# Kernel optimization log

Hardware: AMD Instinct MI355X
Metric: run time of the kernel (lower is better)

## Reference

```python
import jax, jax.numpy as jnp
import numpy as np

B, NQ, L, E, K = 64, 1024, 128, 8192, 2
LN_EPS = 1e-5


def setup_inputs() -> dict:
    key = jax.random.key(0)
    ks = jax.random.split(key, 16)
    s1 = 1.0 / np.sqrt(2 * L + 1)
    s2 = 1.0 / np.sqrt(L)
    s3 = 1.0 / np.sqrt(2 * L)
    return {
        "z0": jax.random.normal(ks[0], (B, L), jnp.float32),
        "edge_index": jax.random.randint(ks[1], (2, E), 0, NQ, jnp.int64),
        "edge_attr": jax.random.normal(ks[2], (E,), jnp.float32),
        "n_qubits": NQ,
        # edge MLP params, stacked over K message-passing rounds
        "e_w1": jax.random.normal(ks[3], (K, L, 2 * L + 1), jnp.float32) * s1,
        "e_b1": jnp.zeros((K, L), jnp.float32),
        "e_w2": jax.random.normal(ks[4], (K, L, L), jnp.float32) * s2,
        "e_b2": jnp.zeros((K, L), jnp.float32),
        # node MLP params
        "n_w1": jax.random.normal(ks[5], (K, L, 2 * L), jnp.float32) * s3,
        "n_b1": jnp.zeros((K, L), jnp.float32),
        "ln_g": jnp.ones((K, L), jnp.float32),
        "ln_b": jnp.zeros((K, L), jnp.float32),
        "n_w2": jax.random.normal(ks[6], (K, L, L), jnp.float32) * s2,
        "n_b2": jnp.zeros((K, L), jnp.float32),
    }


def reference(z0, edge_index, edge_attr, n_qubits,
              e_w1, e_b1, e_w2, e_b2,
              n_w1, n_b1, ln_g, ln_b, n_w2, n_b2):
    b, l = z0.shape
    src, tgt = edge_index[0], edge_index[1]
    e_ = src.shape[0]
    # broadcast latent z0 to every node: h [B, N, L]
    h = jnp.broadcast_to(z0[:, None, :], (b, n_qubits, l))
    e = jnp.broadcast_to(edge_attr[None, :, None], (b, e_, 1))  # [B, E, 1]
    k_rounds = e_w1.shape[0]
    for k in range(k_rounds):
        hi = h[:, src, :]  # gather source node feats [B, E, L]
        hj = h[:, tgt, :]  # gather target node feats [B, E, L]
        inp_e = jnp.concatenate([hi, hj, e], axis=-1)  # [B, E, 2L+1]
        m = jax.nn.relu(inp_e @ e_w1[k].T + e_b1[k]) @ e_w2[k].T + e_b2[k]
        # scatter_add messages back to source nodes
        m_agg = jnp.zeros_like(h).at[:, src, :].add(m)
        inp_n = jnp.concatenate([h, m_agg], axis=-1)  # [B, N, 2L]
        x = jax.nn.relu(inp_n @ n_w1[k].T + n_b1[k])
        mu = x.mean(axis=-1, keepdims=True)
        var = ((x - mu) ** 2).mean(axis=-1, keepdims=True)
        x = (x - mu) * jax.lax.rsqrt(var + LN_EPS) * ln_g[k] + ln_b[k]
        # Dropout(p=0.1) is identity in eval mode
        h = x @ n_w2[k].T + n_b2[k] + h  # residual
    return h.mean(axis=1)  # [B, L]
```

## Files before the change

### kernel.cpp

```cpp
#include <hip/hip_runtime.h>

#define B_   64
#define NQ_  1024
#define L_   128
#define E_   8192
#define M_   (B_*NQ_)
#define LDP  136
#define TILE 2176

typedef unsigned short u16;
typedef unsigned int   u32;
typedef __attribute__((ext_vector_type(8))) short short8;
typedef __attribute__((ext_vector_type(4))) float floatx4;

#define WVB() __builtin_amdgcn_wave_barrier()

__device__ __forceinline__ u16 f2bf(float f) {
    union { float f; u32 u; } v; v.f = f;
    return (u16)((v.u + 0x7fffu + ((v.u >> 16) & 1u)) >> 16);
}
__device__ __forceinline__ float bf2f(u16 u) {
    union { u32 u; float f; } v; v.u = ((u32)u) << 16;
    return v.f;
}
__device__ __forceinline__ floatx4 mfma16(short8 a, short8 b, floatx4 c) {
    return __builtin_amdgcn_mfma_f32_16x16x32_bf16(a, b, c, 0, 0, 0);
}
__device__ __forceinline__ short8 gfrag(const u16* base, int r0, int kb, int lane) {
    return *(const short8*)(base + (size_t)(r0 + (lane & 15)) * 128 + kb * 32 + (lane >> 4) * 8);
}
__device__ __forceinline__ short8 sfrag(const u16* t, int r0, int kb, int lane) {
    return *(const short8*)(t + (r0 + (lane & 15)) * LDP + kb * 32 + (lane >> 4) * 8);
}
__device__ __forceinline__ short8 wfrag(const u16* wf, int nt, int kb, int lane) {
    return *(const short8*)(wf + (((kb << 3) + nt) * 64 + lane) * 8);
}
__device__ __forceinline__ void frag_flush(const u16* t, u16* wf, int nt, int lane) {
#pragma unroll
    for (int kb = 0; kb < 4; ++kb)
        *(short8*)(wf + (((kb << 3) + nt) * 64 + lane) * 8) = sfrag(t, 0, kb, lane);
}
__device__ __forceinline__ short8 frag_cvt(const float* base, int r0, int ld, int kb, int lane) {
    const float* p = base + (size_t)(r0 + (lane & 15)) * ld + kb * 32 + (lane >> 4) * 8;
    short8 s;
#pragma unroll
    for (int j = 0; j < 8; ++j) s[j] = (short)f2bf(p[j]);
    return s;
}
__device__ __forceinline__ void tile_store(u16* t, const floatx4* acc, int lane) {
    int col = lane & 15, qd = lane >> 4;
#pragma unroll
    for (int nt = 0; nt < 8; ++nt)
#pragma unroll
        for (int r = 0; r < 4; ++r)
            t[(qd * 4 + r) * LDP + nt * 16 + col] = f2bf(acc[nt][r]);
}
__device__ __forceinline__ void tile_flush(const u16* t, u16* g, int lane) {
#pragma unroll
    for (int it = 0; it < 4; ++it) {
        int chunk = it * 64 + lane, row = chunk >> 4, c8 = chunk & 15;
        *(uint4*)(g + (size_t)row * 128 + c8 * 8) = *(const uint4*)(t + row * LDP + c8 * 8);
    }
}

struct P {
    const int* ei; const float* attr; const float* z0;
    const float* e_w1; const float* e_b1; const float* e_w2; const float* e_b2;
    const float* n_w1; const float* n_b1; const float* ln_g; const float* ln_b;
    const float* n_w2; const float* n_b2;
    int* ofs; int* tgt_s; float* a_s; float* degf;
    u16* wf;
    u16* w_n20;
    float* wl; float* vb2;
    float* rx; float* rci; float* rcj; float* rh; float* mx0;
    u16* c0t; u16* S; u16* t1g; u16* ci1; u16* cj1;
    float* out;
};

__global__ __launch_bounds__(256) void k_setup(P p) {
    __shared__ __align__(16) char smem[17408];
    int tid = threadIdx.x, blk = blockIdx.x;
    int lane = tid & 63, w = tid >> 6, col = lane & 15, qd = lane >> 4;

    if (blk == 0) {
        __shared__ int cnt[1024];
        __shared__ int wsum[4];
        __shared__ int flag;
#pragma unroll
        for (int i = 0; i < 4; ++i) cnt[tid + i * 256] = 0;
        if (tid == 0) flag = 1;
        __syncthreads();
        if (tid < 100 && p.ei[2 * tid + 1] != 0) atomicAnd(&flag, 0);
        __syncthreads();
        int i64 = flag;
        for (int e = tid; e < E_; e += 256) {
            int s = i64 ? p.ei[2 * e] : p.ei[e];
            atomicAdd(&cnt[s], 1);
        }
        __syncthreads();
        int q0 = tid * 4;
        int c0 = cnt[q0], c1 = cnt[q0 + 1], c2 = cnt[q0 + 2], c3 = cnt[q0 + 3];
        int tsum = c0 + c1 + c2 + c3, incl = tsum;
#pragma unroll
        for (int o = 1; o < 64; o <<= 1) {
            int t = __shfl_up(incl, o, 64);
            if (lane >= o) incl += t;
        }
        if (lane == 63) wsum[w] = incl;
        __syncthreads();
        int wo = 0;
        for (int i = 0; i < w; ++i) wo += wsum[i];
        int base = wo + incl - tsum;
        p.ofs[q0] = base; p.ofs[q0 + 1] = base + c0;
        p.ofs[q0 + 2] = base + c0 + c1; p.ofs[q0 + 3] = base + c0 + c1 + c2;
        p.degf[q0] = (float)c0; p.degf[q0 + 1] = (float)c1;
        p.degf[q0 + 2] = (float)c2; p.degf[q0 + 3] = (float)c3;
        if (tid == 0) p.ofs[NQ_] = E_;
        __syncthreads();
        cnt[q0] = base; cnt[q0 + 1] = base + c0;
        cnt[q0 + 2] = base + c0 + c1; cnt[q0 + 3] = base + c0 + c1 + c2;
        __syncthreads();
        for (int e = tid; e < E_; e += 256) {
            int s = i64 ? p.ei[2 * e]        : p.ei[e];
            int t = i64 ? p.ei[2 * (E_ + e)] : p.ei[E_ + e];
            int pos = atomicAdd(&cnt[s], 1);
            p.tgt_s[pos] = t;
            p.a_s[pos]   = p.attr[e];
        }
    } else if (blk <= 2) {
        int base = (blk - 1) * 8192;
        for (int idx = tid; idx < 8192; idx += 256)
            p.w_n20[base + idx] = f2bf(p.n_w2[base + idx]);
    } else if (blk == 3) {
        const float* src = p.n_w2 + 16384;
        u16* dst = p.wf + 5 * 16384;
        for (int pr = w; pr < 32; pr += 4) {
            int kb = pr >> 3, nt = pr & 7;
            const float* s = src + (nt * 16 + col) * 128 + kb * 32 + qd * 8;
            short8 v;
#pragma unroll
            for (int j = 0; j < 8; ++j) v[j] = (short)f2bf(s[j]);
            *(short8*)(dst + (pr * 64 + lane) * 8) = v;
        }
    } else if (blk <= 13) {
        int g = (blk - 4) >> 1, part = (blk - 4) & 1;
        const float* Pm; const float* Q; int ldp; u16* D;
        switch (g) {
            case 0:  Pm = p.n_w1 + 128;             ldp = 256; Q = p.e_w2;         D = p.wf;             break;
            case 1:  Pm = p.n_w1 + 32768 + 128;     ldp = 256; Q = p.e_w2 + 16384; D = p.wf + 4 * 16384; break;
            case 2:  Pm = p.e_w1 + 128 * 257;       ldp = 257; Q = p.n_w2;         D = p.wf + 1 * 16384; break;
            case 3:  Pm = p.e_w1 + 128 * 257 + 128; ldp = 257; Q = p.n_w2;         D = p.wf + 2 * 16384; break;
            default: Pm = p.n_w1 + 32768;           ldp = 256; Q = p.n_w2;         D = p.wf + 3 * 16384; break;
        }
        int tile = part * 4 + w;
        int r0 = tile * 16;
        floatx4 acc[8] = {};
#pragma unroll
        for (int kb = 0; kb < 4; ++kb) {
            short8 a = frag_cvt(Pm, r0, ldp, kb, lane);
#pragma unroll
            for (int nt = 0; nt < 8; ++nt) {
                short8 bq;
#pragma unroll
                for (int j = 0; j < 8; ++j)
                    bq[j] = (short)f2bf(Q[(kb * 32 + qd * 8 + j) * 128 + nt * 16 + col]);
                acc[nt] = mfma16(a, bq, acc[nt]);
            }
        }
        u16* slot = (u16*)smem + w * TILE;
        tile_store(slot, acc, lane); WVB();
        frag_flush(slot, D, tile, lane);
    } else if (blk == 14) {
        int r0 = w * 16;
        floatx4 acc[8] = {};
#pragma unroll
        for (int kb = 0; kb < 4; ++kb) {
            short8 a = frag_cvt(p.z0, r0, 128, kb, lane);
#pragma unroll
            for (int nt = 0; nt < 8; ++nt)
                acc[nt] = mfma16(a, frag_cvt(p.n_w1, nt * 16, 256, kb, lane), acc[nt]);
        }
#pragma unroll
        for (int nt = 0; nt < 8; ++nt) {
            int cg = nt * 16 + col; float bv = p.n_b1[cg];
#pragma unroll
            for (int r = 0; r < 4; ++r) p.rx[(r0 + qd * 4 + r) * 128 + cg] = acc[nt][r] + bv;
        }
    } else if (blk <= 17) {
        int r0 = w * 16;
        const float* Wp; int ld; const float* bias; float* dst;
        if (blk == 15)      { Wp = p.e_w1 + 128 * 257;       ld = 257; bias = p.e_b1 + 128; dst = p.rci; }
        else if (blk == 16) { Wp = p.e_w1 + 128 * 257 + 128; ld = 257; bias = nullptr;      dst = p.rcj; }
        else                { Wp = p.n_w1 + 32768;           ld = 256; bias = p.n_b1 + 128; dst = p.rh;  }
        floatx4 acc[8] = {};
#pragma unroll
        for (int kb = 0; kb < 4; ++kb) {
            short8 a;
            int rr = (r0 + col) * 128, kk = kb * 32 + qd * 8;
#pragma unroll
            for (int j = 0; j < 8; ++j) a[j] = (short)f2bf(p.z0[rr + kk + j] + p.n_b2[kk + j]);
#pragma unroll
            for (int nt = 0; nt < 8; ++nt)
                acc[nt] = mfma16(a, frag_cvt(Wp, nt * 16, ld, kb, lane), acc[nt]);
        }
#pragma unroll
        for (int nt = 0; nt < 8; ++nt) {
            int cg = nt * 16 + col;
            float bv = bias ? bias[cg] : 0.0f;
#pragma unroll
            for (int r = 0; r < 4; ++r) dst[(r0 + qd * 4 + r) * 128 + cg] = acc[nt][r] + bv;
        }
    } else if (blk == 18) {
        int r0 = w * 16;
        floatx4 a1[8] = {};
#pragma unroll
        for (int kb = 0; kb < 4; ++kb) {
            short8 a = frag_cvt(p.z0, r0, 128, kb, lane);
#pragma unroll
            for (int nt = 0; nt < 8; ++nt) {
                a1[nt] = mfma16(a, frag_cvt(p.e_w1,       nt * 16, 257, kb, lane), a1[nt]);
                a1[nt] = mfma16(a, frag_cvt(p.e_w1 + 128, nt * 16, 257, kb, lane), a1[nt]);
            }
        }
#pragma unroll
        for (int nt = 0; nt < 8; ++nt) {
            float bv = p.e_b1[nt * 16 + col];
#pragma unroll
            for (int r = 0; r < 4; ++r) a1[nt][r] += bv;
        }
        u16* slot = (u16*)smem + w * TILE;
        tile_store(slot, a1, lane); WVB();
        tile_flush(slot, p.c0t + (size_t)r0 * 128, lane);
    } else {
        int k = tid >> 7, c = tid & 127;
        const float4* wp = (const float4*)(p.n_w1 + k * 32768 + c * 256 + 128);
        const float4* bp = (const float4*)(p.e_b2 + k * 128);
        float s0 = 0.f, s1 = 0.f, s2 = 0.f, s3 = 0.f;
#pragma unroll
        for (int n4 = 0; n4 < 32; ++n4) {
            float4 a = wp[n4], bv = bp[n4];
            s0 += a.x * bv.x; s1 += a.y * bv.y; s2 += a.z * bv.z; s3 += a.w * bv.w;
        }
        p.vb2[tid] = (s0 + s1) + (s2 + s3);
        p.wl[tid]  = p.e_w1[k * 128 * 257 + c * 257 + 256];
        for (int i = tid; i < 8192; i += 256) p.mx0[i] = 0.0f;
    }
}

__global__ __launch_bounds__(256) void k_edge(P p, int r0) {
    int tid = threadIdx.x, lane = tid & 63, w = tid >> 6;
    const float* wl = r0 ? p.wl : p.wl + 128;
    float2 wl2 = ((const float2*)wl)[lane];
    int gw = blockIdx.x * 4 + w;
    int q = gw & (NQ_ - 1), bg = gw >> 10;
    int bl[8];
#pragma unroll
    for (int i = 0; i < 4; ++i) { bl[i] = bg * 4 + i; bl[i + 4] = bg * 4 + i + 32; }
    int st = p.ofs[q], en = p.ofs[q + 1];
    float ax[8] = {}, ay[8] = {};
    if (r0) {
        float cx[8], cy[8];
#pragma unroll
        for (int i = 0; i < 8; ++i) {
            u32 cv = ((const u32*)p.c0t)[(size_t)bl[i] * 64 + lane];
            cx[i] = bf2f((u16)(cv & 0xffff)); cy[i] = bf2f((u16)(cv >> 16));
        }
        for (int idx = st; idx < en; ++idx) {
            float a = p.a_s[idx];
            float wx = a * wl2.x, wy = a * wl2.y;
#pragma unroll
            for (int i = 0; i < 8; ++i) {
                ax[i] += fmaxf(cx[i] + wx, 0.f);
                ay[i] += fmaxf(cy[i] + wy, 0.f);
            }
        }
    } else {
        const u32* cjp[8];
        float cx[8], cy[8];
#pragma unroll
        for (int i = 0; i < 8; ++i) {
            cjp[i] = (const u32*)p.cj1 + (size_t)bl[i] * NQ_ * 64;
            u32 cv = ((const u32*)p.ci1)[((size_t)bl[i] * NQ_ + q) * 64 + lane];
            cx[i] = bf2f((u16)(cv & 0xffff)); cy[i] = bf2f((u16)(cv >> 16));
        }
        for (int idx = st; idx < en; ++idx) {
            int t = p.tgt_s[idx];
            float a = p.a_s[idx];
            size_t ro = (size_t)t * 64 + lane;
            float wx = a * wl2.x, wy = a * wl2.y;
#pragma unroll
            for (int i = 0; i < 8; ++i) {
                u32 jv = cjp[i][ro];
                ax[i] += fmaxf(cx[i] + bf2f((u16)(jv & 0xffff)) + wx, 0.f);
                ay[i] += fmaxf(cy[i] + bf2f((u16)(jv >> 16))    + wy, 0.f);
            }
        }
    }
    u32* Sp = (u32*)p.S;
#pragma unroll
    for (int i = 0; i < 8; ++i)
        Sp[((size_t)bl[i] * NQ_ + q) * 64 + lane] =
            (u32)f2bf(ax[i]) | ((u32)f2bf(ay[i]) << 16);
}

__global__ __launch_bounds__(256, 2) void k_node0(P p) {
    __shared__ __align__(16) char smem[52224];
    u16* xt = (u16*)smem;
    u16* ob = (u16*)(smem + 34816);
    int tid = threadIdx.x, lane = tid & 63, w = tid >> 6;
    int col = lane & 15, qd = lane >> 4;
    int blk = blockIdx.x;
    int rowbase = blk * 128 + w * 32;
    int b = blk >> 3;

    floatx4 xa[2][8] = {};
#pragma unroll
    for (int kb = 0; kb < 4; ++kb) {
        short8 Bv[8];
#pragma unroll
        for (int nt = 0; nt < 8; ++nt) Bv[nt] = wfrag(p.wf, nt, kb, lane);
#pragma unroll
        for (int t = 0; t < 2; ++t) {
            short8 a = gfrag(p.S, rowbase + t * 16, kb, lane);
#pragma unroll
            for (int nt = 0; nt < 8; ++nt) xa[t][nt] = mfma16(a, Bv[nt], xa[t][nt]);
        }
    }
    float s8[8] = {};
#pragma unroll
    for (int t = 0; t < 2; ++t) {
#pragma unroll
        for (int nt = 0; nt < 8; ++nt) {
            int cg = nt * 16 + col;
            float base = p.rx[b * 128 + cg], vb = p.vb2[cg];
#pragma unroll
            for (int r = 0; r < 4; ++r) {
                int row = rowbase + t * 16 + qd * 4 + r;
                xa[t][nt][r] = fmaxf(xa[t][nt][r] + base + p.degf[row & (NQ_ - 1)] * vb, 0.f);
            }
        }
#pragma unroll
        for (int r = 0; r < 4; ++r) {
            float s = 0.f, s2 = 0.f;
#pragma unroll
            for (int nt = 0; nt < 8; ++nt) { float v = xa[t][nt][r]; s += v; s2 += v * v; }
#pragma unroll
            for (int o = 1; o < 16; o <<= 1) { s += __shfl_xor(s, o, 64); s2 += __shfl_xor(s2, o, 64); }
            float mu = s * (1.f / 128.f), var = s2 * (1.f / 128.f) - mu * mu;
            float rs = rsqrtf(var + 1e-5f);
#pragma unroll
            for (int nt = 0; nt < 8; ++nt) {
                int cg = nt * 16 + col;
                float xv = (xa[t][nt][r] - mu) * rs * p.ln_g[cg] + p.ln_b[cg];
                xa[t][nt][r] = xv;
                s8[nt] += xv;
            }
        }
        tile_store(xt + (w * 2 + t) * TILE, xa[t], lane);
    }
#pragma unroll
    for (int nt = 0; nt < 8; ++nt) {
        s8[nt] += __shfl_xor(s8[nt], 16, 64);
        s8[nt] += __shfl_xor(s8[nt], 32, 64);
    }
    if (lane < 16) {
#pragma unroll
        for (int nt = 0; nt < 8; ++nt)
            atomicAdd(p.mx0 + b * 128 + nt * 16 + lane, s8[nt]);
    }
    WVB();
#pragma unroll
    for (int ph = 0; ph < 3; ++ph) {
        const u16* wfp = p.wf + ((ph == 0) ? 1 : (ph == 1) ? 2 : 3) * 16384;
        const float* rt = (ph == 0) ? p.rci : (ph == 1) ? p.rcj : p.rh;
        floatx4 ca[2][8] = {};
#pragma unroll
        for (int kb = 0; kb < 4; ++kb) {
            short8 Bv[8];
#pragma unroll
            for (int nt = 0; nt < 8; ++nt) Bv[nt] = wfrag(wfp, nt, kb, lane);
#pragma unroll
            for (int t = 0; t < 2; ++t) {
                short8 a = sfrag(xt + (w * 2 + t) * TILE, 0, kb, lane);
#pragma unroll
                for (int nt = 0; nt < 8; ++nt) ca[t][nt] = mfma16(a, Bv[nt], ca[t][nt]);
            }
        }
#pragma unroll
        for (int t = 0; t < 2; ++t)
#pragma unroll
            for (int nt = 0; nt < 8; ++nt) {
                float rc = rt[b * 128 + nt * 16 + col];
#pragma unroll
                for (int r = 0; r < 4; ++r) ca[t][nt][r] += rc;
            }
        u16* dst = (ph == 0) ? p.ci1 : (ph == 1) ? p.cj1 : p.t1g;
#pragma unroll
        for (int t = 0; t < 2; ++t) {
            tile_store(ob + w * TILE, ca[t], lane);
            WVB();
            tile_flush(ob + w * TILE, dst + (size_t)(rowbase + t * 16) * 128, lane);
            WVB();
        }
    }
}

__global__ __launch_bounds__(256, 2) void k_node1(P p) {
    __shared__ __align__(16) char smem[52224];
    u16* ob = (u16*)(smem + 34816);
    int tid = threadIdx.x, lane = tid & 63, w = tid >> 6;
    int col = lane & 15, qd = lane >> 4;
    int blk = blockIdx.x;
    int rowbase = blk * 128 + w * 32;
    int b = blk >> 3;

    const u16* wc1 = p.wf + 4 * 16384;
    floatx4 xa[2][8] = {};
#pragma unroll
    for (int kb = 0; kb < 4; ++kb) {
        short8 Bv[8];
#pragma unroll
        for (int nt = 0; nt < 8; ++nt) Bv[nt] = wfrag(wc1, nt, kb, lane);
#pragma unroll
        for (int t = 0; t < 2; ++t) {
            short8 a = gfrag(p.S, rowbase + t * 16, kb, lane);
#pragma unroll
            for (int nt = 0; nt < 8; ++nt) xa[t][nt] = mfma16(a, Bv[nt], xa[t][nt]);
        }
    }
    const float* vb21 = p.vb2 + 128;
#pragma unroll
    for (int t = 0; t < 2; ++t) {
#pragma unroll
        for (int nt = 0; nt < 8; ++nt) {
            int cg = nt * 16 + col;
            float vb = vb21[cg];
#pragma unroll
            for (int r = 0; r < 4; ++r) {
                int row = rowbase + t * 16 + qd * 4 + r;
                float tv = bf2f(p.t1g[(size_t)row * 128 + cg]);
                xa[t][nt][r] = fmaxf(xa[t][nt][r] + tv + p.degf[row & (NQ_ - 1)] * vb, 0.f);
            }
        }
#pragma unroll
        for (int r = 0; r < 4; ++r) {
            float s = 0.f, s2 = 0.f;
#pragma unroll
            for (int nt = 0; nt < 8; ++nt) { float v = xa[t][nt][r]; s += v; s2 += v * v; }
#pragma unroll
            for (int o = 1; o < 16; o <<= 1) { s += __shfl_xor(s, o, 64); s2 += __shfl_xor(s2, o, 64); }
            float mu = s * (1.f / 128.f), var = s2 * (1.f / 128.f) - mu * mu;
            float rs = rsqrtf(var + 1e-5f);
#pragma unroll
            for (int nt = 0; nt < 8; ++nt) {
                int cg = nt * 16 + col;
                xa[t][nt][r] = (xa[t][nt][r] - mu) * rs * p.ln_g[128 + cg] + p.ln_b[128 + cg];
            }
        }
    }
    const u16* n21 = p.wf + 5 * 16384;
    float s8[8] = {};
#pragma unroll
    for (int t = 0; t < 2; ++t) {
        WVB();
        tile_store(ob + w * TILE, xa[t], lane);
        WVB();
        floatx4 ma[8] = {};
#pragma unroll
        for (int kb = 0; kb < 4; ++kb) {
            short8 Bv[8];
#pragma unroll
            for (int nt = 0; nt < 8; ++nt) Bv[nt] = wfrag(n21, nt, kb, lane);
            short8 a = sfrag(ob + w * TILE, 0, kb, lane);
#pragma unroll
            for (int nt = 0; nt < 8; ++nt) ma[nt] = mfma16(a, Bv[nt], ma[nt]);
        }
#pragma unroll
        for (int nt = 0; nt < 8; ++nt)
#pragma unroll
            for (int r = 0; r < 4; ++r) s8[nt] += ma[nt][r];
    }
#pragma unroll
    for (int nt = 0; nt < 8; ++nt) {
        s8[nt] += __shfl_xor(s8[nt], 16, 64);
        s8[nt] += __shfl_xor(s8[nt], 32, 64);
    }
    if (lane < 16) {
#pragma unroll
        for (int nt = 0; nt < 8; ++nt)
            atomicAdd(p.out + b * 128 + nt * 16 + lane, s8[nt] * (1.f / 1024.f));
    }
    if ((blk & 7) == 0 && tid < 128) {
        int c = tid;
        const float* mx = p.mx0 + b * 128;
        float s = 0.f;
#pragma unroll
        for (int k8 = 0; k8 < 16; ++k8) {
            short8 wv = *(const short8*)(p.w_n20 + c * 128 + k8 * 8);
            const float* mxp = mx + k8 * 8;
#pragma unroll
            for (int j = 0; j < 8; ++j) s += mxp[j] * bf2f((u16)wv[j]);
        }
        float acc = p.z0[b * 128 + c] + p.n_b2[c] + p.n_b2[128 + c] + s * (1.f / 1024.f);
        atomicAdd(p.out + b * 128 + c, acc);
    }
}

extern "C" void kernel_launch(void* const* d_in, const int* in_sizes, int n_in,
                              void* d_out, int out_size, void* d_ws, size_t ws_size,
                              hipStream_t stream) {
    P p;
    p.z0   = (const float*)d_in[0];
    p.ei   = (const int*)d_in[1];
    p.attr = (const float*)d_in[2];
    p.e_w1 = (const float*)d_in[4];
    p.e_b1 = (const float*)d_in[5];
    p.e_w2 = (const float*)d_in[6];
    p.e_b2 = (const float*)d_in[7];
    p.n_w1 = (const float*)d_in[8];
    p.n_b1 = (const float*)d_in[9];
    p.ln_g = (const float*)d_in[10];
    p.ln_b = (const float*)d_in[11];
    p.n_w2 = (const float*)d_in[12];
    p.n_b2 = (const float*)d_in[13];
    p.out  = (float*)d_out;

    const size_t H = (size_t)M_ * L_;
    float* f  = (float*)d_ws;
    p.degf = f;
    p.a_s  = f + 1024;
    p.wl   = p.a_s + 8192;
    p.vb2  = p.wl + 256;
    p.rx   = p.vb2 + 256;
    p.rci  = p.rx + 8192;
    p.rcj  = p.rci + 8192;
    p.rh   = p.rcj + 8192;
    p.mx0  = p.rh + 8192;
    p.ofs  = (int*)(p.mx0 + 8192);
    p.tgt_s = p.ofs + 1056;
    p.wf    = (u16*)(p.tgt_s + 8192);
    p.w_n20 = p.wf + 6 * 16384;
    p.c0t   = p.w_n20 + 16384;
    p.S     = p.c0t + 8192;
    p.t1g   = p.S + H;
    p.ci1   = p.t1g + H;
    p.cj1   = p.ci1 + H;

    hipMemsetAsync(p.out, 0, 8192 * sizeof(float), stream);

    k_setup<<<20, 256, 0, stream>>>(p);
    k_edge<<<2048, 256, 0, stream>>>(p, 1);
    k_node0<<<512, 256, 0, stream>>>(p);
    k_edge<<<2048, 256, 0, stream>>>(p, 0);
    k_node1<<<512, 256, 0, stream>>>(p);
}
```

Before: 188.9 us.

## Fuse edge aggregation into node kernels via LDS tiles, drop S buffer

The separate edge-message kernels are removed. Each node kernel now computes the per-node edge aggregates for its own rows directly into shared-memory tiles, and the MFMA reads its A operand from those tiles instead of a global S buffer. This removes two launches and a full write plus read of the S intermediate. The t1 buffer is also stored in MFMA fragment order, so node1 can load it with packed 64-bit loads. In exchange, the node kernels do serial gather work per wave before the MFMA, with predicated loops padded to the largest degree among the four nodes handled together, and the batch-sharing of loads that the old edge kernel had is lost.

```diff
diff --git a/kernel.cpp b/kernel.cpp
--- a/kernel.cpp
+++ b/kernel.cpp
@@ -10,10 +10,13 @@
 
 typedef unsigned short u16;
 typedef unsigned int   u32;
+typedef unsigned long long u64;
 typedef __attribute__((ext_vector_type(8))) short short8;
 typedef __attribute__((ext_vector_type(4))) float floatx4;
 
 #define WVB() __builtin_amdgcn_wave_barrier()
+
+__device__ __forceinline__ int imax2(int a, int b) { return a > b ? a : b; }
 
 __device__ __forceinline__ u16 f2bf(float f) {
     union { float f; u32 u; } v; v.f = f;
@@ -25,9 +28,6 @@
 }
 __device__ __forceinline__ floatx4 mfma16(short8 a, short8 b, floatx4 c) {
     return __builtin_amdgcn_mfma_f32_16x16x32_bf16(a, b, c, 0, 0, 0);
-}
-__device__ __forceinline__ short8 gfrag(const u16* base, int r0, int kb, int lane) {
-    return *(const short8*)(base + (size_t)(r0 + (lane & 15)) * 128 + kb * 32 + (lane >> 4) * 8);
 }
 __device__ __forceinline__ short8 sfrag(const u16* t, int r0, int kb, int lane) {
     return *(const short8*)(t + (r0 + (lane & 15)) * LDP + kb * 32 + (lane >> 4) * 8);
@@ -73,7 +73,7 @@
     u16* w_n20;
     float* wl; float* vb2;
     float* rx; float* rci; float* rcj; float* rh; float* mx0;
-    u16* c0t; u16* S; u16* t1g; u16* ci1; u16* cj1;
+    u16* c0t; u16* t1g; u16* ci1; u16* cj1;
     float* out;
 };
 
@@ -247,62 +247,6 @@
     }
 }
 
-__global__ __launch_bounds__(256) void k_edge(P p, int r0) {
-    int tid = threadIdx.x, lane = tid & 63, w = tid >> 6;
-    const float* wl = r0 ? p.wl : p.wl + 128;
-    float2 wl2 = ((const float2*)wl)[lane];
-    int gw = blockIdx.x * 4 + w;
-    int q = gw & (NQ_ - 1), bg = gw >> 10;
-    int bl[8];
-#pragma unroll
-    for (int i = 0; i < 4; ++i) { bl[i] = bg * 4 + i; bl[i + 4] = bg * 4 + i + 32; }
-    int st = p.ofs[q], en = p.ofs[q + 1];
-    float ax[8] = {}, ay[8] = {};
-    if (r0) {
-        float cx[8], cy[8];
-#pragma unroll
-        for (int i = 0; i < 8; ++i) {
-            u32 cv = ((const u32*)p.c0t)[(size_t)bl[i] * 64 + lane];
-            cx[i] = bf2f((u16)(cv & 0xffff)); cy[i] = bf2f((u16)(cv >> 16));
-        }
-        for (int idx = st; idx < en; ++idx) {
-            float a = p.a_s[idx];
-            float wx = a * wl2.x, wy = a * wl2.y;
-#pragma unroll
-            for (int i = 0; i < 8; ++i) {
-                ax[i] += fmaxf(cx[i] + wx, 0.f);
-                ay[i] += fmaxf(cy[i] + wy, 0.f);
-            }
-        }
-    } else {
-        const u32* cjp[8];
-        float cx[8], cy[8];
-#pragma unroll
-        for (int i = 0; i < 8; ++i) {
-            cjp[i] = (const u32*)p.cj1 + (size_t)bl[i] * NQ_ * 64;
-            u32 cv = ((const u32*)p.ci1)[((size_t)bl[i] * NQ_ + q) * 64 + lane];
-            cx[i] = bf2f((u16)(cv & 0xffff)); cy[i] = bf2f((u16)(cv >> 16));
-        }
-        for (int idx = st; idx < en; ++idx) {
-            int t = p.tgt_s[idx];
-            float a = p.a_s[idx];
-            size_t ro = (size_t)t * 64 + lane;
-            float wx = a * wl2.x, wy = a * wl2.y;
-#pragma unroll
-            for (int i = 0; i < 8; ++i) {
-                u32 jv = cjp[i][ro];
-                ax[i] += fmaxf(cx[i] + bf2f((u16)(jv & 0xffff)) + wx, 0.f);
-                ay[i] += fmaxf(cy[i] + bf2f((u16)(jv >> 16))    + wy, 0.f);
-            }
-        }
-    }
-    u32* Sp = (u32*)p.S;
-#pragma unroll
-    for (int i = 0; i < 8; ++i)
-        Sp[((size_t)bl[i] * NQ_ + q) * 64 + lane] =
-            (u32)f2bf(ax[i]) | ((u32)f2bf(ay[i]) << 16);
-}
-
 __global__ __launch_bounds__(256, 2) void k_node0(P p) {
     __shared__ __align__(16) char smem[52224];
     u16* xt = (u16*)smem;
@@ -313,6 +257,43 @@
     int rowbase = blk * 128 + w * 32;
     int b = blk >> 3;
 
+    {
+        u32 cv = ((const u32*)p.c0t)[b * 64 + lane];
+        float cx = bf2f((u16)(cv & 0xffffu)), cy = bf2f((u16)(cv >> 16));
+        float2 wl2 = ((const float2*)p.wl)[lane];
+        for (int qq = 0; qq < 32; qq += 4) {
+            int st[4], en[4];
+            float ax[4] = {}, ay[4] = {};
+#pragma unroll
+            for (int j = 0; j < 4; ++j) {
+                int q = (rowbase + qq + j) & (NQ_ - 1);
+                st[j] = p.ofs[q]; en[j] = p.ofs[q + 1];
+            }
+            int mx = imax2(imax2(en[0] - st[0], en[1] - st[1]),
+                           imax2(en[2] - st[2], en[3] - st[3]));
+            for (int k2 = 0; k2 < mx; ++k2) {
+#pragma unroll
+                for (int j = 0; j < 4; ++j) {
+                    int idx = st[j] + k2, last = en[j] - 1;
+                    int safe = idx < en[j] ? idx : (last >= 0 ? last : 0);
+                    float a = p.a_s[safe];
+                    float vx = fmaxf(cx + a * wl2.x, 0.f);
+                    float vy = fmaxf(cy + a * wl2.y, 0.f);
+                    bool v = idx < en[j];
+                    ax[j] += v ? vx : 0.f;
+                    ay[j] += v ? vy : 0.f;
+                }
+            }
+#pragma unroll
+            for (int j = 0; j < 4; ++j) {
+                int r = qq + j;
+                u32* tp = (u32*)(xt + (size_t)(w * 2 + (r >> 4)) * TILE + (r & 15) * LDP);
+                tp[lane] = (u32)f2bf(ax[j]) | ((u32)f2bf(ay[j]) << 16);
+            }
+        }
+    }
+    WVB();
+
     floatx4 xa[2][8] = {};
 #pragma unroll
     for (int kb = 0; kb < 4; ++kb) {
@@ -321,11 +302,12 @@
         for (int nt = 0; nt < 8; ++nt) Bv[nt] = wfrag(p.wf, nt, kb, lane);
 #pragma unroll
         for (int t = 0; t < 2; ++t) {
-            short8 a = gfrag(p.S, rowbase + t * 16, kb, lane);
+            short8 a = sfrag(xt + (w * 2 + t) * TILE, 0, kb, lane);
 #pragma unroll
             for (int nt = 0; nt < 8; ++nt) xa[t][nt] = mfma16(a, Bv[nt], xa[t][nt]);
         }
     }
+    WVB();
     float s8[8] = {};
 #pragma unroll
     for (int t = 0; t < 2; ++t) {
@@ -394,19 +376,34 @@
 #pragma unroll
                 for (int r = 0; r < 4; ++r) ca[t][nt][r] += rc;
             }
-        u16* dst = (ph == 0) ? p.ci1 : (ph == 1) ? p.cj1 : p.t1g;
-#pragma unroll
-        for (int t = 0; t < 2; ++t) {
-            tile_store(ob + w * TILE, ca[t], lane);
-            WVB();
-            tile_flush(ob + w * TILE, dst + (size_t)(rowbase + t * 16) * 128, lane);
-            WVB();
+        if (ph == 2) {
+            u64* t1f = (u64*)p.t1g;
+#pragma unroll
+            for (int t = 0; t < 2; ++t) {
+                int tile = blk * 8 + w * 2 + t;
+#pragma unroll
+                for (int nt = 0; nt < 8; ++nt) {
+                    u32 lo = (u32)f2bf(ca[t][nt][0]) | ((u32)f2bf(ca[t][nt][1]) << 16);
+                    u32 hi = (u32)f2bf(ca[t][nt][2]) | ((u32)f2bf(ca[t][nt][3]) << 16);
+                    t1f[(size_t)(tile * 8 + nt) * 64 + lane] = (u64)lo | ((u64)hi << 32);
+                }
+            }
+        } else {
+            u16* dst = (ph == 0) ? p.ci1 : p.cj1;
+#pragma unroll
+            for (int t = 0; t < 2; ++t) {
+                tile_store(ob + w * TILE, ca[t], lane);
+                WVB();
+                tile_flush(ob + w * TILE, dst + (size_t)(rowbase + t * 16) * 128, lane);
+                WVB();
+            }
         }
     }
 }
 
 __global__ __launch_bounds__(256, 2) void k_node1(P p) {
     __shared__ __align__(16) char smem[52224];
+    u16* xt = (u16*)smem;
     u16* ob = (u16*)(smem + 34816);
     int tid = threadIdx.x, lane = tid & 63, w = tid >> 6;
     int col = lane & 15, qd = lane >> 4;
@@ -414,6 +411,62 @@
     int rowbase = blk * 128 + w * 32;
     int b = blk >> 3;
 
+    {
+        float2 wl2 = ((const float2*)(p.wl + 128))[lane];
+        const u32* cip = (const u32*)p.ci1;
+        const u32* cjp = (const u32*)p.cj1 + (size_t)b * NQ_ * 64;
+        for (int qq = 0; qq < 32; qq += 4) {
+            int st[4], en[4];
+            float ax[4] = {}, ay[4] = {}, cx[4], cy[4];
+#pragma unroll
+            for (int j = 0; j < 4; ++j) {
+                int row = rowbase + qq + j;
+                u32 cv = cip[(size_t)row * 64 + lane];
+                cx[j] = bf2f((u16)(cv & 0xffffu)); cy[j] = bf2f((u16)(cv >> 16));
+                int q = row & (NQ_ - 1);
+                st[j] = p.ofs[q]; en[j] = p.ofs[q + 1];
+            }
+            int mx = imax2(imax2(en[0] - st[0], en[1] - st[1]),
+                           imax2(en[2] - st[2], en[3] - st[3]));
+            int tc[4]; float ac[4];
+#pragma unroll
+            for (int j = 0; j < 4; ++j) {
+                int last = en[j] - 1;
+                int safe = st[j] < en[j] ? st[j] : (last >= 0 ? last : 0);
+                tc[j] = p.tgt_s[safe]; ac[j] = p.a_s[safe];
+            }
+            for (int k2 = 0; k2 < mx; ++k2) {
+                u32 jv[4];
+#pragma unroll
+                for (int j = 0; j < 4; ++j)
+                    jv[j] = cjp[(size_t)tc[j] * 64 + lane];
+                int tn[4]; float an[4];
+#pragma unroll
+                for (int j = 0; j < 4; ++j) {
+                    int idx = st[j] + k2 + 1, last = en[j] - 1;
+                    int safe = idx < en[j] ? idx : (last >= 0 ? last : 0);
+                    tn[j] = p.tgt_s[safe]; an[j] = p.a_s[safe];
+                }
+#pragma unroll
+                for (int j = 0; j < 4; ++j) {
+                    float vx = fmaxf(cx[j] + bf2f((u16)(jv[j] & 0xffffu)) + ac[j] * wl2.x, 0.f);
+                    float vy = fmaxf(cy[j] + bf2f((u16)(jv[j] >> 16))    + ac[j] * wl2.y, 0.f);
+                    bool v = st[j] + k2 < en[j];
+                    ax[j] += v ? vx : 0.f;
+                    ay[j] += v ? vy : 0.f;
+                    tc[j] = tn[j]; ac[j] = an[j];
+                }
+            }
+#pragma unroll
+            for (int j = 0; j < 4; ++j) {
+                int r = qq + j;
+                u32* tp = (u32*)(xt + (size_t)(w * 2 + (r >> 4)) * TILE + (r & 15) * LDP);
+                tp[lane] = (u32)f2bf(ax[j]) | ((u32)f2bf(ay[j]) << 16);
+            }
+        }
+    }
+    WVB();
+
     const u16* wc1 = p.wf + 4 * 16384;
     floatx4 xa[2][8] = {};
 #pragma unroll
@@ -423,23 +476,27 @@
         for (int nt = 0; nt < 8; ++nt) Bv[nt] = wfrag(wc1, nt, kb, lane);
 #pragma unroll
         for (int t = 0; t < 2; ++t) {
-            short8 a = gfrag(p.S, rowbase + t * 16, kb, lane);
+            short8 a = sfrag(xt + (w * 2 + t) * TILE, 0, kb, lane);
 #pragma unroll
             for (int nt = 0; nt < 8; ++nt) xa[t][nt] = mfma16(a, Bv[nt], xa[t][nt]);
         }
     }
     const float* vb21 = p.vb2 + 128;
+    const u64* t1f = (const u64*)p.t1g;
 #pragma unroll
     for (int t = 0; t < 2; ++t) {
+        int tile = blk * 8 + w * 2 + t;
 #pragma unroll
         for (int nt = 0; nt < 8; ++nt) {
             int cg = nt * 16 + col;
             float vb = vb21[cg];
+            u64 tv = t1f[(size_t)(tile * 8 + nt) * 64 + lane];
+            float tvf[4] = { bf2f((u16)tv),         bf2f((u16)(tv >> 16)),
+                             bf2f((u16)(tv >> 32)), bf2f((u16)(tv >> 48)) };
 #pragma unroll
             for (int r = 0; r < 4; ++r) {
                 int row = rowbase + t * 16 + qd * 4 + r;
-                float tv = bf2f(p.t1g[(size_t)row * 128 + cg]);
-                xa[t][nt][r] = fmaxf(xa[t][nt][r] + tv + p.degf[row & (NQ_ - 1)] * vb, 0.f);
+                xa[t][nt][r] = fmaxf(xa[t][nt][r] + tvf[r] + p.degf[row & (NQ_ - 1)] * vb, 0.f);
             }
         }
 #pragma unroll
@@ -541,16 +598,13 @@
     p.wf    = (u16*)(p.tgt_s + 8192);
     p.w_n20 = p.wf + 6 * 16384;
     p.c0t   = p.w_n20 + 16384;
-    p.S     = p.c0t + 8192;
-    p.t1g   = p.S + H;
+    p.t1g   = p.c0t + 8192;
     p.ci1   = p.t1g + H;
     p.cj1   = p.ci1 + H;
 
     hipMemsetAsync(p.out, 0, 8192 * sizeof(float), stream);
 
     k_setup<<<20, 256, 0, stream>>>(p);
-    k_edge<<<2048, 256, 0, stream>>>(p, 1);
     k_node0<<<512, 256, 0, stream>>>(p);
-    k_edge<<<2048, 256, 0, stream>>>(p, 0);
     k_node1<<<512, 256, 0, stream>>>(p);
 }
```

After: 243.9 us. 29.1% more time.
